# Performance work log

Measured on AMD Instinct MI355X. Metric: run time of the kernel, lower is better.

The kernel has to match this reference:

```python
import jax, jax.numpy as jnp
import numpy as np

N_PATHS = 8
T2_EFF = 0.5 * 100.0 + 0.5 * (100 // 50)  # p_dimer*T2_dimer + p_trimer*T2_trimer = 51.0
J_FREQ = 20.0


def setup_inputs() -> dict:
    key = jax.random.key(0)
    ks = jax.random.split(key, 5)
    B, D, H, P = 2048, 1024, 1024, N_PATHS
    return {
        "x": jax.random.normal(ks[0], (B, D), dtype=jnp.float32),
        "W_input": jax.random.normal(ks[1], (D, H), dtype=jnp.float32) * 0.1,
        "W_paths": jax.random.normal(ks[2], (P, H, H), dtype=jnp.float32) * 0.1,
        "J_coupling": jax.random.normal(ks[3], (P, P), dtype=jnp.float32) * 0.01,
        "coherent_state": jax.random.normal(ks[4], (B, P, H), dtype=jnp.float32),
        "t": jnp.ones((1,), dtype=jnp.float32),  # time_since_formation buffer
    }


def reference(x, W_input, W_paths, J_coupling, coherent_state, t):
    # base activation: [B, H]
    base = x @ W_input
    # all per-path matmuls batched into one einsum: [B, P, H]
    path_act = jnp.einsum("bh,phk->bpk", base, W_paths)
    # coherence decay gate (scalar, broadcasts)
    alpha = jnp.clip(jnp.exp(-t[0] / T2_EFF), 0.0, 1.0)
    superposition = alpha * coherent_state + (1.0 - alpha) * path_act
    # interference matrix from symmetrized J-coupling
    J_sym = 0.5 * (J_coupling + J_coupling.T)
    phase = 2.0 * jnp.pi * J_FREQ * t[0] / 1000.0
    interference = jax.nn.softmax(jnp.cos(phase * J_sym), axis=1)  # [P, P]
    # double-loop mixing == small matmul over path dim
    interfered = jnp.einsum("ij,bjh->bih", interference, superposition) / N_PATHS
    interfered = interfered * alpha  # coherence_factor == alpha
    # no measurement (default path): mean over paths
    return jnp.mean(interfered, axis=1)  # [B, H]
```

## Files before the change

### kernel.cpp

```cpp
#include <hip/hip_runtime.h>
#include <cstdint>


typedef __attribute__((ext_vector_type(8))) __bf16 bf16x8;
typedef __attribute__((ext_vector_type(4))) float f32x4;

__device__ __forceinline__ unsigned short f32_to_bf16_rne(float f) {
  unsigned int u = __float_as_uint(f);
  u += 0x7fffu + ((u >> 16) & 1u);
  return (unsigned short)(u >> 16);
}

__device__ __forceinline__ void load16_lds(const void* g, void* l) {
  __builtin_amdgcn_global_load_lds(
      (const __attribute__((address_space(1))) void*)g,
      (__attribute__((address_space(3))) void*)(unsigned int)(unsigned long long)l,
      16, 0, 0);
}

__global__ void k_scalars(const float* __restrict__ J, const float* __restrict__ t,
                          float* __restrict__ s) {
  const int lane = threadIdx.x;
  float tv = t[0];
  float alpha = expf(-tv / 51.0f);
  alpha = fminf(fmaxf(alpha, 0.0f), 1.0f);
  float phase = 2.0f * 3.14159265358979323846f * 20.0f * tv / 1000.0f;
  int i = lane >> 3, j = lane & 7;
  float jsym = 0.5f * (J[i * 8 + j] + J[j * 8 + i]);
  float e = expf(cosf(phase * jsym));
  float rs = e;
  rs += __shfl_xor(rs, 1);
  rs += __shfl_xor(rs, 2);
  rs += __shfl_xor(rs, 4);
  float p = e / rs;
  float cs = p;
  cs += __shfl_xor(cs, 8);
  cs += __shfl_xor(cs, 16);
  cs += __shfl_xor(cs, 32);
  float w = alpha * (1.0f / 64.0f) * cs;
  if (lane < 8) {
    s[lane] = w * (1.0f - alpha);
    s[8 + lane] = w * alpha;
  }
}

__global__ void k_convert(const float* __restrict__ x, const float* __restrict__ win,
                          unsigned short* __restrict__ xb, unsigned short* __restrict__ winb) {
  int idx = blockIdx.x * 256 + threadIdx.x;
  const float4* src;
  unsigned short* dst;
  int off;
  if (idx < 524288) { src = (const float4*)x;   dst = xb;   off = idx; }
  else              { src = (const float4*)win; dst = winb; off = idx - 524288; }
  float4 v = src[off];
  ushort4 o;
  o.x = f32_to_bf16_rne(v.x);
  o.y = f32_to_bf16_rne(v.y);
  o.z = f32_to_bf16_rne(v.z);
  o.w = f32_to_bf16_rne(v.w);
  ((ushort4*)dst)[off] = o;
}

__global__ void k_wefft(const float* __restrict__ Wp, const float* __restrict__ s,
                        unsigned short* __restrict__ wefft) {
  __shared__ float lt[32][33];
  const int tx = threadIdx.x;
  const int ty = threadIdx.y;
  const int k0 = blockIdx.x * 32;
  const int h0 = blockIdx.y * 32;
  float wj[8];
#pragma unroll
  for (int j = 0; j < 8; j++) wj[j] = s[j];
  float acc[4] = {0.f, 0.f, 0.f, 0.f};
#pragma unroll
  for (int j = 0; j < 8; j++) {
    const float* base = Wp + (size_t)j * 1024 * 1024;
#pragma unroll
    for (int r = 0; r < 4; r++) {
      int h1 = h0 + ty + 8 * r;
      acc[r] += wj[j] * base[(size_t)h1 * 1024 + k0 + tx];
    }
  }
#pragma unroll
  for (int r = 0; r < 4; r++) lt[ty + 8 * r][tx] = acc[r];
  __syncthreads();
#pragma unroll
  for (int r = 0; r < 4; r++) {
    float v = lt[tx][ty + 8 * r];
    wefft[(size_t)(k0 + ty + 8 * r) * 1024 + h0 + tx] = f32_to_bf16_rne(v);
  }
}

template <int MAIN>
__global__ __launch_bounds__(256) void k_gemm64(
    const unsigned short* __restrict__ A,
    const unsigned short* __restrict__ B,
    int K,
    float* __restrict__ outf,
    unsigned short* __restrict__ outb,
    const float* __restrict__ coh,
    const float* __restrict__ s) {
  __shared__ alignas(16) unsigned short As[64 * 32];
  __shared__ alignas(16) unsigned short Bs[64 * 32];
  const int m0 = blockIdx.x * 64;
  const int n0 = blockIdx.y * 64;
  const int tid = threadIdx.x;
  const int wave = tid >> 6;
  const int lane = tid & 63;
  const int quad = lane >> 4;
  const int t16 = lane & 15;

  const int srow = lane >> 2;
  const int sgrp = (lane & 3) ^ (srow & 3);
  const unsigned short* gA = A + (size_t)(m0 + wave * 16 + srow) * K + sgrp * 8;
  const unsigned short* gB = B + (size_t)(n0 + wave * 16 + srow) * K + sgrp * 8;
  unsigned short* lA = As + wave * 512 + lane * 8;
  unsigned short* lB = Bs + wave * 512 + lane * 8;

  const int wm = (wave >> 1) * 32;
  const int wn = (wave & 1) * 32;
  const int ar0 = wm + t16, ar1 = wm + 16 + t16;
  const int br0 = wn + t16, br1 = wn + 16 + t16;
  const unsigned short* pa0 = As + ar0 * 32 + ((quad ^ (ar0 & 3)) * 8);
  const unsigned short* pa1 = As + ar1 * 32 + ((quad ^ (ar1 & 3)) * 8);
  const unsigned short* pb0 = Bs + br0 * 32 + ((quad ^ (br0 & 3)) * 8);
  const unsigned short* pb1 = Bs + br1 * 32 + ((quad ^ (br1 & 3)) * 8);

  f32x4 acc00 = {0.f, 0.f, 0.f, 0.f}, acc01 = acc00, acc10 = acc00, acc11 = acc00;

  for (int kt = 0; kt < K; kt += 32) {
    __syncthreads();
    load16_lds(gA + kt, lA);
    load16_lds(gB + kt, lB);
    __syncthreads();
    bf16x8 a0 = *(const bf16x8*)pa0;
    bf16x8 a1 = *(const bf16x8*)pa1;
    bf16x8 b0 = *(const bf16x8*)pb0;
    bf16x8 b1 = *(const bf16x8*)pb1;
    acc00 = __builtin_amdgcn_mfma_f32_16x16x32_bf16(a0, b0, acc00, 0, 0, 0);
    acc01 = __builtin_amdgcn_mfma_f32_16x16x32_bf16(a0, b1, acc01, 0, 0, 0);
    acc10 = __builtin_amdgcn_mfma_f32_16x16x32_bf16(a1, b0, acc10, 0, 0, 0);
    acc11 = __builtin_amdgcn_mfma_f32_16x16x32_bf16(a1, b1, acc11, 0, 0, 0);
  }

  f32x4 accv[2][2] = {{acc00, acc01}, {acc10, acc11}};
  if constexpr (MAIN != 0) {
    float wA[8];
#pragma unroll
    for (int p = 0; p < 8; p++) wA[p] = s[8 + p];
#pragma unroll
    for (int i = 0; i < 2; i++) {
#pragma unroll
      for (int r = 0; r < 4; r++) {
        int m = m0 + wm + i * 16 + quad * 4 + r;
        const float* cb = coh + (size_t)m * 8192;
#pragma unroll
        for (int j = 0; j < 2; j++) {
          int n = n0 + wn + j * 16 + t16;
          float c = 0.f;
#pragma unroll
          for (int p = 0; p < 8; p++) c += wA[p] * cb[p * 1024 + n];
          outf[(size_t)m * 1024 + n] = accv[i][j][r] + c;
        }
      }
    }
  } else {
#pragma unroll
    for (int i = 0; i < 2; i++) {
#pragma unroll
      for (int r = 0; r < 4; r++) {
        int m = m0 + wm + i * 16 + quad * 4 + r;
#pragma unroll
        for (int j = 0; j < 2; j++) {
          int n = n0 + wn + j * 16 + t16;
          outb[(size_t)m * 1024 + n] = f32_to_bf16_rne(accv[i][j][r]);
        }
      }
    }
  }
}

extern "C" void kernel_launch(void* const* d_in, const int* in_sizes, int n_in,
                              void* d_out, int out_size, void* d_ws, size_t ws_size,
                              hipStream_t stream) {
  const float* x   = (const float*)d_in[0];
  const float* win = (const float*)d_in[1];
  const float* wp  = (const float*)d_in[2];
  const float* J   = (const float*)d_in[3];
  const float* coh = (const float*)d_in[4];
  const float* t   = (const float*)d_in[5];
  float* out = (float*)d_out;

  char* ws = (char*)d_ws;
  float* s              = (float*)ws;
  unsigned short* xb    = (unsigned short*)(ws + 64);
  unsigned short* winb  = (unsigned short*)(ws + 64 + 4u * 1024 * 1024);
  unsigned short* wefft = (unsigned short*)(ws + 64 + 6u * 1024 * 1024);
  unsigned short* wct   = (unsigned short*)(ws + 64 + 8u * 1024 * 1024);

  k_scalars<<<1, 64, 0, stream>>>(J, t, s);
  k_convert<<<3072, 256, 0, stream>>>(x, win, xb, winb);
  k_wefft<<<dim3(32, 32), dim3(32, 8), 0, stream>>>(wp, s, wefft);
  k_gemm64<0><<<dim3(16, 16), 256, 0, stream>>>(wefft, winb, 1024, nullptr, wct,
                                                nullptr, s);
  k_gemm64<1><<<dim3(32, 16), 256, 0, stream>>>(xb, wct, 1024, out, nullptr,
                                                coh, s);
}
```

Before: 182.5 us.

## Merge prep kernels into one launch and move coherent-state term out of GEMM epilogue

Folds the scalar, convert and weight-reduction kernels into a single k_prep launch. Each wave recomputes the softmax scalars itself instead of reading them from a separate kernel. The coherent-state weighted sum is now computed in prep with vectorized loads and written to the output, so the main GEMM epilogue only does a read-add-write. The GEMM is retiled to 64x32 blocks with BK=64 and an 8-way XOR swizzle, which doubles the block count for occupancy and halves the number of barriers per K. The cost is an extra read-modify-write of the output and some redundant scalar computation.

New measurement: 162.3 us. 11.1% less time.

```diff
diff --git a/kernel.cpp b/kernel.cpp
--- a/kernel.cpp
+++ b/kernel.cpp
@@ -18,12 +18,12 @@
       16, 0, 0);
 }
 
-__global__ void k_scalars(const float* __restrict__ J, const float* __restrict__ t,
-                          float* __restrict__ s) {
-  const int lane = threadIdx.x;
+__device__ __forceinline__ void wave_scalars(const float* __restrict__ J,
+                                             const float* __restrict__ t,
+                                             float* w_out, float* alpha_out) {
+  const int lane = threadIdx.x & 63;
   float tv = t[0];
-  float alpha = expf(-tv / 51.0f);
-  alpha = fminf(fmaxf(alpha, 0.0f), 1.0f);
+  float alpha = fminf(fmaxf(expf(-tv / 51.0f), 0.0f), 1.0f);
   float phase = 2.0f * 3.14159265358979323846f * 20.0f * tv / 1000.0f;
   int i = lane >> 3, j = lane & 7;
   float jsym = 0.5f * (J[i * 8 + j] + J[j * 8 + i]);
@@ -37,144 +37,165 @@
   cs += __shfl_xor(cs, 8);
   cs += __shfl_xor(cs, 16);
   cs += __shfl_xor(cs, 32);
-  float w = alpha * (1.0f / 64.0f) * cs;
-  if (lane < 8) {
-    s[lane] = w * (1.0f - alpha);
-    s[8 + lane] = w * alpha;
-  }
-}
-
-__global__ void k_convert(const float* __restrict__ x, const float* __restrict__ win,
-                          unsigned short* __restrict__ xb, unsigned short* __restrict__ winb) {
-  int idx = blockIdx.x * 256 + threadIdx.x;
-  const float4* src;
-  unsigned short* dst;
-  int off;
-  if (idx < 524288) { src = (const float4*)x;   dst = xb;   off = idx; }
-  else              { src = (const float4*)win; dst = winb; off = idx - 524288; }
-  float4 v = src[off];
-  ushort4 o;
-  o.x = f32_to_bf16_rne(v.x);
-  o.y = f32_to_bf16_rne(v.y);
-  o.z = f32_to_bf16_rne(v.z);
-  o.w = f32_to_bf16_rne(v.w);
-  ((ushort4*)dst)[off] = o;
-}
-
-__global__ void k_wefft(const float* __restrict__ Wp, const float* __restrict__ s,
-                        unsigned short* __restrict__ wefft) {
-  __shared__ float lt[32][33];
-  const int tx = threadIdx.x;
-  const int ty = threadIdx.y;
-  const int k0 = blockIdx.x * 32;
-  const int h0 = blockIdx.y * 32;
-  float wj[8];
-#pragma unroll
-  for (int j = 0; j < 8; j++) wj[j] = s[j];
-  float acc[4] = {0.f, 0.f, 0.f, 0.f};
-#pragma unroll
-  for (int j = 0; j < 8; j++) {
-    const float* base = Wp + (size_t)j * 1024 * 1024;
-#pragma unroll
-    for (int r = 0; r < 4; r++) {
-      int h1 = h0 + ty + 8 * r;
-      acc[r] += wj[j] * base[(size_t)h1 * 1024 + k0 + tx];
-    }
-  }
-#pragma unroll
-  for (int r = 0; r < 4; r++) lt[ty + 8 * r][tx] = acc[r];
-  __syncthreads();
-#pragma unroll
-  for (int r = 0; r < 4; r++) {
-    float v = lt[tx][ty + 8 * r];
-    wefft[(size_t)(k0 + ty + 8 * r) * 1024 + h0 + tx] = f32_to_bf16_rne(v);
+  *w_out = alpha * (1.0f / 64.0f) * cs;
+  *alpha_out = alpha;
+}
+
+__global__ __launch_bounds__(256, 4) void k_prep(
+    const float* __restrict__ x, const float* __restrict__ win,
+    const float* __restrict__ wp, const float* __restrict__ J,
+    const float* __restrict__ t, const float* __restrict__ coh,
+    unsigned short* __restrict__ xb, unsigned short* __restrict__ winb,
+    unsigned short* __restrict__ wefft, float* __restrict__ out) {
+  const int blk = blockIdx.x;
+  const int tid = threadIdx.x;
+  const int lane = tid & 63;
+
+  if (blk < 3072) {
+    int idx = blk * 256 + tid;
+    const float4* src;
+    unsigned short* dst;
+    int off;
+    if (idx < 524288) { src = (const float4*)x;   dst = xb;   off = idx; }
+    else              { src = (const float4*)win; dst = winb; off = idx - 524288; }
+    float4 v = src[off];
+    ushort4 o;
+    o.x = f32_to_bf16_rne(v.x);
+    o.y = f32_to_bf16_rne(v.y);
+    o.z = f32_to_bf16_rne(v.z);
+    o.w = f32_to_bf16_rne(v.w);
+    ((ushort4*)dst)[off] = o;
+  } else if (blk < 5120) {
+    float wv, alpha;
+    wave_scalars(J, t, &wv, &alpha);
+    float wHI[8];
+#pragma unroll
+    for (int p = 0; p < 8; p++) wHI[p] = __shfl(wv, (lane & 56) | p) * alpha;
+    int idx = (blk - 3072) * 256 + tid;
+    int b = idx >> 8, hq = idx & 255;
+    const f32x4* cb = (const f32x4*)(coh + (size_t)b * 8192) + hq;
+    f32x4 acc = {0.f, 0.f, 0.f, 0.f};
+#pragma unroll
+    for (int p = 0; p < 8; p++) acc += wHI[p] * cb[p * 256];
+    ((f32x4*)out)[idx] = acc;
+  } else {
+    __shared__ float lt[64][69];
+    float wv, alpha;
+    wave_scalars(J, t, &wv, &alpha);
+    float wLO[8];
+#pragma unroll
+    for (int p = 0; p < 8; p++)
+      wLO[p] = __shfl(wv, (lane & 56) | p) * (1.0f - alpha);
+    const int q = blk - 5120;
+    const int a0 = (q & 15) * 64;
+    const int b0 = (q >> 4) * 64;
+    const int rb = tid >> 4, c = tid & 15;
+    f32x4 acc[4];
+#pragma unroll
+    for (int s = 0; s < 4; s++) acc[s] = {0.f, 0.f, 0.f, 0.f};
+#pragma unroll
+    for (int j = 0; j < 8; j++) {
+      const float* base = wp + (size_t)j * 1024 * 1024 + b0 + c * 4;
+      float wj = wLO[j];
+#pragma unroll
+      for (int s = 0; s < 4; s++) {
+        f32x4 v = *(const f32x4*)(base + (size_t)(a0 + rb + 16 * s) * 1024);
+        acc[s] += wj * v;
+      }
+    }
+#pragma unroll
+    for (int s = 0; s < 4; s++)
+#pragma unroll
+      for (int e = 0; e < 4; e++) lt[rb + 16 * s][c * 4 + e] = acc[s][e];
+    __syncthreads();
+    const int h2l = tid >> 2, h1g = (tid & 3) * 16;
+    unsigned short* dst = wefft + (size_t)(b0 + h2l) * 1024 + a0 + h1g;
+#pragma unroll
+    for (int v4 = 0; v4 < 4; v4++) {
+      ushort4 o;
+      o.x = f32_to_bf16_rne(lt[h1g + v4 * 4 + 0][h2l]);
+      o.y = f32_to_bf16_rne(lt[h1g + v4 * 4 + 1][h2l]);
+      o.z = f32_to_bf16_rne(lt[h1g + v4 * 4 + 2][h2l]);
+      o.w = f32_to_bf16_rne(lt[h1g + v4 * 4 + 3][h2l]);
+      ((ushort4*)dst)[v4] = o;
+    }
   }
 }
 
 template <int MAIN>
-__global__ __launch_bounds__(256) void k_gemm64(
-    const unsigned short* __restrict__ A,
-    const unsigned short* __restrict__ B,
-    int K,
-    float* __restrict__ outf,
-    unsigned short* __restrict__ outb,
-    const float* __restrict__ coh,
-    const float* __restrict__ s) {
-  __shared__ alignas(16) unsigned short As[64 * 32];
-  __shared__ alignas(16) unsigned short Bs[64 * 32];
+__global__ __launch_bounds__(256, 4) void k_gemm(
+    const unsigned short* __restrict__ A, const unsigned short* __restrict__ B,
+    float* __restrict__ outf, unsigned short* __restrict__ outb) {
+  constexpr int K = 1024;
+  constexpr int BK = 64;
+  __shared__ alignas(16) unsigned short As[64 * BK];
+  __shared__ alignas(16) unsigned short Bs[32 * BK];
+
   const int m0 = blockIdx.x * 64;
-  const int n0 = blockIdx.y * 64;
+  const int n0 = blockIdx.y * 32;
   const int tid = threadIdx.x;
   const int wave = tid >> 6;
   const int lane = tid & 63;
   const int quad = lane >> 4;
   const int t16 = lane & 15;
 
-  const int srow = lane >> 2;
-  const int sgrp = (lane & 3) ^ (srow & 3);
-  const unsigned short* gA = A + (size_t)(m0 + wave * 16 + srow) * K + sgrp * 8;
-  const unsigned short* gB = B + (size_t)(n0 + wave * 16 + srow) * K + sgrp * 8;
-  unsigned short* lA = As + wave * 512 + lane * 8;
-  unsigned short* lB = Bs + wave * 512 + lane * 8;
-
-  const int wm = (wave >> 1) * 32;
-  const int wn = (wave & 1) * 32;
-  const int ar0 = wm + t16, ar1 = wm + 16 + t16;
-  const int br0 = wn + t16, br1 = wn + 16 + t16;
-  const unsigned short* pa0 = As + ar0 * 32 + ((quad ^ (ar0 & 3)) * 8);
-  const unsigned short* pa1 = As + ar1 * 32 + ((quad ^ (ar1 & 3)) * 8);
-  const unsigned short* pb0 = Bs + br0 * 32 + ((quad ^ (br0 & 3)) * 8);
-  const unsigned short* pb1 = Bs + br1 * 32 + ((quad ^ (br1 & 3)) * 8);
-
-  f32x4 acc00 = {0.f, 0.f, 0.f, 0.f}, acc01 = acc00, acc10 = acc00, acc11 = acc00;
-
-  for (int kt = 0; kt < K; kt += 32) {
+  const int crow = lane >> 3;
+  const int grp = lane & 7;
+  const unsigned short* gA[2];
+  unsigned short* lA[2];
+#pragma unroll
+  for (int c = 0; c < 2; c++) {
+    int r = wave * 16 + c * 8 + crow;
+    gA[c] = A + (size_t)(m0 + r) * K + (size_t)((grp ^ (r & 7)) * 8);
+    lA[c] = As + (wave * 16 + c * 8) * BK + lane * 8;
+  }
+  const int rB = wave * 8 + crow;
+  const unsigned short* gB = B + (size_t)(n0 + rB) * K + (size_t)((grp ^ (rB & 7)) * 8);
+  unsigned short* lB = Bs + (wave * 8) * BK + lane * 8;
+
+  const int ra = wave * 16 + t16;
+  const unsigned short* pa[2];
+  const unsigned short* pb[2][2];
+#pragma unroll
+  for (int kk = 0; kk < 2; kk++)
+    pa[kk] = As + ra * BK + ((kk * 4 + quad) ^ (ra & 7)) * 8;
+#pragma unroll
+  for (int ni = 0; ni < 2; ni++) {
+    int rb = ni * 16 + t16;
+#pragma unroll
+    for (int kk = 0; kk < 2; kk++)
+      pb[ni][kk] = Bs + rb * BK + ((kk * 4 + quad) ^ (rb & 7)) * 8;
+  }
+
+  f32x4 acc[2] = {{0.f, 0.f, 0.f, 0.f}, {0.f, 0.f, 0.f, 0.f}};
+
+  for (int kt = 0; kt < K; kt += BK) {
     __syncthreads();
-    load16_lds(gA + kt, lA);
+    load16_lds(gA[0] + kt, lA[0]);
+    load16_lds(gA[1] + kt, lA[1]);
     load16_lds(gB + kt, lB);
     __syncthreads();
-    bf16x8 a0 = *(const bf16x8*)pa0;
-    bf16x8 a1 = *(const bf16x8*)pa1;
-    bf16x8 b0 = *(const bf16x8*)pb0;
-    bf16x8 b1 = *(const bf16x8*)pb1;
-    acc00 = __builtin_amdgcn_mfma_f32_16x16x32_bf16(a0, b0, acc00, 0, 0, 0);
-    acc01 = __builtin_amdgcn_mfma_f32_16x16x32_bf16(a0, b1, acc01, 0, 0, 0);
-    acc10 = __builtin_amdgcn_mfma_f32_16x16x32_bf16(a1, b0, acc10, 0, 0, 0);
-    acc11 = __builtin_amdgcn_mfma_f32_16x16x32_bf16(a1, b1, acc11, 0, 0, 0);
-  }
-
-  f32x4 accv[2][2] = {{acc00, acc01}, {acc10, acc11}};
-  if constexpr (MAIN != 0) {
-    float wA[8];
-#pragma unroll
-    for (int p = 0; p < 8; p++) wA[p] = s[8 + p];
-#pragma unroll
-    for (int i = 0; i < 2; i++) {
-#pragma unroll
-      for (int r = 0; r < 4; r++) {
-        int m = m0 + wm + i * 16 + quad * 4 + r;
-        const float* cb = coh + (size_t)m * 8192;
-#pragma unroll
-        for (int j = 0; j < 2; j++) {
-          int n = n0 + wn + j * 16 + t16;
-          float c = 0.f;
-#pragma unroll
-          for (int p = 0; p < 8; p++) c += wA[p] * cb[p * 1024 + n];
-          outf[(size_t)m * 1024 + n] = accv[i][j][r] + c;
-        }
-      }
-    }
-  } else {
-#pragma unroll
-    for (int i = 0; i < 2; i++) {
-#pragma unroll
-      for (int r = 0; r < 4; r++) {
-        int m = m0 + wm + i * 16 + quad * 4 + r;
-#pragma unroll
-        for (int j = 0; j < 2; j++) {
-          int n = n0 + wn + j * 16 + t16;
-          outb[(size_t)m * 1024 + n] = f32_to_bf16_rne(accv[i][j][r]);
-        }
+#pragma unroll
+    for (int kk = 0; kk < 2; kk++) {
+      bf16x8 a = *(const bf16x8*)pa[kk];
+      bf16x8 b0v = *(const bf16x8*)pb[0][kk];
+      bf16x8 b1v = *(const bf16x8*)pb[1][kk];
+      acc[0] = __builtin_amdgcn_mfma_f32_16x16x32_bf16(a, b0v, acc[0], 0, 0, 0);
+      acc[1] = __builtin_amdgcn_mfma_f32_16x16x32_bf16(a, b1v, acc[1], 0, 0, 0);
+    }
+  }
+
+#pragma unroll
+  for (int r = 0; r < 4; r++) {
+    const int m = m0 + wave * 16 + quad * 4 + r;
+#pragma unroll
+    for (int ni = 0; ni < 2; ni++) {
+      const int n = n0 + ni * 16 + t16;
+      const size_t idx = (size_t)m * 1024 + n;
+      if constexpr (MAIN) {
+        outf[idx] = outf[idx] + acc[ni][r];
+      } else {
+        outb[idx] = f32_to_bf16_rne(acc[ni][r]);
       }
     }
   }
@@ -192,17 +213,12 @@
   float* out = (float*)d_out;
 
   char* ws = (char*)d_ws;
-  float* s              = (float*)ws;
-  unsigned short* xb    = (unsigned short*)(ws + 64);
-  unsigned short* winb  = (unsigned short*)(ws + 64 + 4u * 1024 * 1024);
-  unsigned short* wefft = (unsigned short*)(ws + 64 + 6u * 1024 * 1024);
-  unsigned short* wct   = (unsigned short*)(ws + 64 + 8u * 1024 * 1024);
-
-  k_scalars<<<1, 64, 0, stream>>>(J, t, s);
-  k_convert<<<3072, 256, 0, stream>>>(x, win, xb, winb);
-  k_wefft<<<dim3(32, 32), dim3(32, 8), 0, stream>>>(wp, s, wefft);
-  k_gemm64<0><<<dim3(16, 16), 256, 0, stream>>>(wefft, winb, 1024, nullptr, wct,
-                                                nullptr, s);
-  k_gemm64<1><<<dim3(32, 16), 256, 0, stream>>>(xb, wct, 1024, out, nullptr,
-                                                coh, s);
-}
+  unsigned short* xb    = (unsigned short*)ws;
+  unsigned short* winb  = (unsigned short*)(ws + 4u * 1024 * 1024);
+  unsigned short* wefft = (unsigned short*)(ws + 6u * 1024 * 1024);
+  unsigned short* wct   = (unsigned short*)(ws + 8u * 1024 * 1024);
+
+  k_prep<<<5376, 256, 0, stream>>>(x, win, wp, J, t, coh, xb, winb, wefft, out);
+  k_gemm<0><<<dim3(16, 32), 256, 0, stream>>>(wefft, winb, nullptr, wct);
+  k_gemm<1><<<dim3(32, 32), 256, 0, stream>>>(xb, wct, out, nullptr);
+}
```
